# Kernel optimization log

Measured on AMD Instinct MI355X. Metric: run time of the kernel, lower is better.

Reference implementation:

```python
import jax, jax.numpy as jnp
import numpy as np

SHAPES = ((80, 80), (40, 40), (20, 20), (10, 10))  # (H, W) per level
N_HEADS = 8
N_POINTS = 4
D_MODEL = 512  # double_d_model = 2*256 (densefusion=True)
D_FFN = 1024
B = 2
L = len(SHAPES)
S = sum(h * w for h, w in SHAPES)  # 8500
EPS = 1e-5


def _layernorm(x, g, b):
    m = jnp.mean(x, axis=-1, keepdims=True)
    v = jnp.mean((x - m) ** 2, axis=-1, keepdims=True)
    return (x - m) * jax.lax.rsqrt(v + EPS) * g + b


def _reference_points(shapes):
    # encoder get_reference_points with valid_ratios == 1 -> [S, 2] (x, y) in (0,1)
    refs = []
    for (H, W) in shapes:
        ry = (jnp.arange(H, dtype=jnp.float32) + 0.5) / H
        rx = (jnp.arange(W, dtype=jnp.float32) + 0.5) / W
        gy, gx = jnp.meshgrid(ry, rx, indexing='ij')
        refs.append(jnp.stack([gx.reshape(-1), gy.reshape(-1)], axis=-1))
    return jnp.concatenate(refs, axis=0)


def _sample_level(val, loc, H, W):
    # val: [B, H*W, h, d]; loc: [B, S, h, P, 2] normalized in [0,1]
    b, _, h, d = val.shape
    s, p = loc.shape[1], loc.shape[3]
    x = loc[..., 0] * W - 0.5
    y = loc[..., 1] * H - 0.5
    x0 = jnp.floor(x)
    y0 = jnp.floor(y)
    wx = x - x0
    wy = y - y0
    x0i = x0.astype(jnp.int32)
    y0i = y0.astype(jnp.int32)

    def gather(xi, yi):
        valid = ((xi >= 0) & (xi < W) & (yi >= 0) & (yi < H)).astype(val.dtype)
        idx = jnp.clip(yi, 0, H - 1) * W + jnp.clip(xi, 0, W - 1)  # [B,S,h,P]
        idx2 = jnp.transpose(idx, (0, 1, 3, 2)).reshape(b, s * p, h)  # [B,S*P,h]
        g = jnp.take_along_axis(val, idx2[..., None], axis=1)  # [B,S*P,h,d]
        vmask = jnp.transpose(valid, (0, 1, 3, 2))[..., None]  # [B,S,P,h,1]
        return g.reshape(b, s, p, h, d) * vmask

    v00 = gather(x0i, y0i)
    v01 = gather(x0i + 1, y0i)
    v10 = gather(x0i, y0i + 1)
    v11 = gather(x0i + 1, y0i + 1)
    wxT = jnp.transpose(wx, (0, 1, 3, 2))[..., None]
    wyT = jnp.transpose(wy, (0, 1, 3, 2))[..., None]
    return (v00 * (1 - wxT) * (1 - wyT) + v01 * wxT * (1 - wyT)
            + v10 * (1 - wxT) * wyT + v11 * wxT * wyT)  # [B,S,P,h,d]


def _forward(src, pos, w_off, b_off, w_attn, b_attn, w_val, b_val, w_out, b_out,
             ln1_g, ln1_b, w1, b1, w2, b2, ln2_g, ln2_b, shapes):
    b, s, c = src.shape
    h, p, l = N_HEADS, N_POINTS, len(shapes)
    d = c // h
    q = src + pos
    value = (src @ w_val + b_val).reshape(b, s, h, d)
    offsets = (q @ w_off + b_off).reshape(b, s, h, l, p, 2)
    attn = jax.nn.softmax((q @ w_attn + b_attn).reshape(b, s, h, l * p), axis=-1)
    attn = attn.reshape(b, s, h, l, p)
    ref = _reference_points(shapes)  # [S,2]
    # offset normalizer = (W_l, H_l)
    norm = jnp.array([[W, H] for (H, W) in shapes], dtype=src.dtype)  # [L,2]
    loc = ref[None, :, None, None, None, :] + offsets / norm[None, None, None, :, None, :]
    # split value per level and sample
    starts = np.cumsum([0] + [H * W for (H, W) in shapes])[:-1]
    sampled = []
    for lvl, (H, W) in enumerate(shapes):
        val_l = jax.lax.dynamic_slice_in_dim(value, int(starts[lvl]), H * W, axis=1)
        sampled.append(_sample_level(val_l, loc[:, :, :, lvl], H, W))
    sampled = jnp.stack(sampled)  # [L,B,S,P,h,d]
    out = jnp.einsum('lbqphd,bqhlp->bqhd', sampled, attn).reshape(b, s, c)
    attn_out = out @ w_out + b_out
    x = _layernorm(src + attn_out, ln1_g, ln1_b)
    ffn = jax.nn.relu(x @ w1 + b1) @ w2 + b2
    return _layernorm(x + ffn, ln2_g, ln2_b)


def setup_inputs() -> dict:
    key = jax.random.key(0)
    ks = jax.random.split(key, 20)
    sc = 0.02
    C = D_MODEL
    hLP = N_HEADS * L * N_POINTS
    f32 = jnp.float32
    inp = {
        'src': jax.random.normal(ks[0], (B, S, C), f32),
        'pos': jax.random.normal(ks[1], (B, S, C), f32),
        'w_off': jax.random.normal(ks[2], (C, hLP * 2), f32) * sc,
        'b_off': jax.random.normal(ks[3], (hLP * 2,), f32) * sc,
        'w_attn': jax.random.normal(ks[4], (C, hLP), f32) * sc,
        'b_attn': jax.random.normal(ks[5], (hLP,), f32) * sc,
        'w_val': jax.random.normal(ks[6], (C, C), f32) * sc,
        'b_val': jnp.zeros((C,), f32),
        'w_out': jax.random.normal(ks[7], (C, C), f32) * sc,
        'b_out': jnp.zeros((C,), f32),
        'ln1_g': jnp.ones((C,), f32),
        'ln1_b': jnp.zeros((C,), f32),
        'w1': jax.random.normal(ks[8], (C, D_FFN), f32) * sc,
        'b1': jnp.zeros((D_FFN,), f32),
        'w2': jax.random.normal(ks[9], (D_FFN, C), f32) * sc,
        'b2': jnp.zeros((C,), f32),
        'ln2_g': jnp.ones((C,), f32),
        'ln2_b': jnp.zeros((C,), f32),
        'spatial_shapes': jnp.array(SHAPES, dtype=jnp.int32),
    }
    return inp


def reference(src, pos, w_off, b_off, w_attn, b_attn, w_val, b_val, w_out, b_out,
              ln1_g, ln1_b, w1, b1, w2, b2, ln2_g, ln2_b, spatial_shapes):
    shapes = tuple((int(a), int(b)) for a, b in np.asarray(spatial_shapes))
    return _forward(src, pos, w_off, b_off, w_attn, b_attn, w_val, b_val, w_out, b_out,
                    ln1_g, ln1_b, w1, b1, w2, b2, ln2_g, ln2_b, shapes)
```

## Files before the change

### kernel.cpp

```cpp
#include <hip/hip_runtime.h>


typedef __bf16 bf16_t;
typedef __bf16 bf16x8 __attribute__((ext_vector_type(8)));
typedef __bf16 bf16x4 __attribute__((ext_vector_type(4)));
typedef float  f32x4  __attribute__((ext_vector_type(4)));

#define M_ROWS 17000
#define S_LEN  8500

__device__ inline void store_c(float* p, float v)  { *p = v; }
__device__ inline void store_c(bf16_t* p, float v) { *p = (bf16_t)v; }

__device__ inline float4 load4f(const float* p)  { return *(const float4*)p; }
__device__ inline float4 load4f(const bf16_t* p) {
    bf16x4 v = *(const bf16x4*)p;
    return make_float4((float)v[0], (float)v[1], (float)v[2], (float)v[3]);
}

__global__ __launch_bounds__(256)
void transpose_kernel(const float* __restrict__ in, bf16_t* __restrict__ out,
                      int K, int N) {
    __shared__ float s[32][33];
    int tx = threadIdx.x & 31, ty = threadIdx.x >> 5;
    int k0 = blockIdx.x * 32, n0 = blockIdx.y * 32;
    #pragma unroll
    for (int i = 0; i < 4; i++)
        s[ty + 8 * i][tx] = in[(size_t)(k0 + ty + 8 * i) * N + n0 + tx];
    __syncthreads();
    #pragma unroll
    for (int i = 0; i < 4; i++)
        out[(size_t)(n0 + ty + 8 * i) * K + k0 + tx] = (bf16_t)s[tx][ty + 8 * i];
}

__global__ __launch_bounds__(384)
void prep_bias_kernel(const float* __restrict__ b_off, const float* __restrict__ b_attn,
                      float* __restrict__ bias_oa) {
    int i = threadIdx.x;
    bias_oa[i] = (i < 256) ? b_off[i] : b_attn[i - 256];
}

__global__ __launch_bounds__(256)
void add_q_kernel(const float* __restrict__ a, const float* __restrict__ b,
                  bf16_t* __restrict__ q, bf16_t* __restrict__ src_bf, int n4) {
    int i = blockIdx.x * 256 + threadIdx.x;
    if (i >= n4) return;
    float4 av = *(const float4*)(a + (size_t)i * 4);
    float4 bv = *(const float4*)(b + (size_t)i * 4);
    bf16x4 sv, ov;
    sv[0] = (bf16_t)av.x; sv[1] = (bf16_t)av.y; sv[2] = (bf16_t)av.z; sv[3] = (bf16_t)av.w;
    ov[0] = (bf16_t)(av.x + bv.x);
    ov[1] = (bf16_t)(av.y + bv.y);
    ov[2] = (bf16_t)(av.z + bv.z);
    ov[3] = (bf16_t)(av.w + bv.w);
    *(bf16x4*)(q      + (size_t)i * 4) = ov;
    *(bf16x4*)(src_bf + (size_t)i * 4) = sv;
}

template<typename OT, bool RELU>
__global__ __launch_bounds__(256)
void gemm128_kernel(const bf16_t* __restrict__ A, const bf16_t* __restrict__ Wt,
                    const float* __restrict__ bias, OT* __restrict__ Cout,
                    int M, int N, int K) {
    __shared__ bf16_t As[2][128][40];
    __shared__ bf16_t Bs[2][128][40];

    const int tid  = threadIdx.x;
    const int wave = tid >> 6;
    const int lane = tid & 63;
    const int quad = lane >> 4;
    const int lq   = lane & 15;
    const int wr   = (wave >> 1) * 64;
    const int wc   = (wave & 1) * 64;
    const int row0 = blockIdx.x * 128;
    const int col0 = blockIdx.y * 128;

    const int sr = tid >> 2;
    const int sc = (tid & 3) * 8;

    const bf16_t* gA0 = A  + (size_t)min(row0 + sr,      M - 1) * K + sc;
    const bf16_t* gA1 = A  + (size_t)min(row0 + sr + 64, M - 1) * K + sc;
    const bf16_t* gB0 = Wt + (size_t)(col0 + sr) * K + sc;
    const bf16_t* gB1 = Wt + (size_t)(col0 + sr + 64) * K + sc;

    f32x4 acc[4][4];
    #pragma unroll
    for (int i = 0; i < 4; i++)
        #pragma unroll
        for (int j = 0; j < 4; j++)
            #pragma unroll
            for (int r = 0; r < 4; r++) acc[i][j][r] = 0.f;

    bf16x8 pa0 = *(const bf16x8*)gA0;
    bf16x8 pa1 = *(const bf16x8*)gA1;
    bf16x8 pb0 = *(const bf16x8*)gB0;
    bf16x8 pb1 = *(const bf16x8*)gB1;

    const int nIter = K >> 5;
    for (int it = 0; it < nIter; it++) {
        const int cur = it & 1;
        *(bf16x8*)&As[cur][sr][sc]      = pa0;
        *(bf16x8*)&As[cur][sr + 64][sc] = pa1;
        *(bf16x8*)&Bs[cur][sr][sc]      = pb0;
        *(bf16x8*)&Bs[cur][sr + 64][sc] = pb1;
        __syncthreads();

        if (it + 1 < nIter) {
            int ko = (it + 1) << 5;
            pa0 = *(const bf16x8*)(gA0 + ko);
            pa1 = *(const bf16x8*)(gA1 + ko);
            pb0 = *(const bf16x8*)(gB0 + ko);
            pb1 = *(const bf16x8*)(gB1 + ko);
        }

        bf16x8 af[4], bfr[4];
        #pragma unroll
        for (int i = 0; i < 4; i++)
            af[i] = *(const bf16x8*)&As[cur][wr + i * 16 + lq][quad * 8];
        #pragma unroll
        for (int j = 0; j < 4; j++)
            bfr[j] = *(const bf16x8*)&Bs[cur][wc + j * 16 + lq][quad * 8];
        #pragma unroll
        for (int i = 0; i < 4; i++)
            #pragma unroll
            for (int j = 0; j < 4; j++)
                acc[i][j] = __builtin_amdgcn_mfma_f32_16x16x32_bf16(af[i], bfr[j], acc[i][j], 0, 0, 0);
    }

    #pragma unroll
    for (int j = 0; j < 4; j++) {
        int col = col0 + wc + j * 16 + lq;
        float bcol = bias[col];
        #pragma unroll
        for (int i = 0; i < 4; i++) {
            int rowb = row0 + wr + i * 16 + quad * 4;
            #pragma unroll
            for (int r = 0; r < 4; r++) {
                int row = rowb + r;
                if (row < M) {
                    float v = acc[i][j][r] + bcol;
                    if (RELU) v = fmaxf(v, 0.f);
                    store_c(Cout + (size_t)row * N + col, v);
                }
            }
        }
    }
}

__global__ __launch_bounds__(256)
void softmax16_kernel(float* __restrict__ oa, int ngroups) {
    int i = blockIdx.x * 256 + threadIdx.x;
    if (i >= ngroups) return;
    float* p = oa + (size_t)(i >> 3) * 384 + 256 + (i & 7) * 16;
    float v[16];
    float4* p4 = (float4*)p;
    #pragma unroll
    for (int j = 0; j < 4; j++) {
        float4 t = p4[j];
        v[4*j+0] = t.x; v[4*j+1] = t.y; v[4*j+2] = t.z; v[4*j+3] = t.w;
    }
    float mx = v[0];
    #pragma unroll
    for (int j = 1; j < 16; j++) mx = fmaxf(mx, v[j]);
    float sm = 0.f;
    #pragma unroll
    for (int j = 0; j < 16; j++) { v[j] = __expf(v[j] - mx); sm += v[j]; }
    float inv = 1.f / sm;
    #pragma unroll
    for (int j = 0; j < 4; j++)
        p4[j] = make_float4(v[4*j]*inv, v[4*j+1]*inv, v[4*j+2]*inv, v[4*j+3]*inv);
}

__global__ __launch_bounds__(256)
void sample_kernel(const bf16_t* __restrict__ value, const float* __restrict__ oa,
                   bf16_t* __restrict__ out) {
    int gw   = blockIdx.x * 4 + (threadIdx.x >> 6);
    int lane = threadIdx.x & 63;
    if (gw >= 2 * S_LEN * 8) return;
    int h  = gw & 7;
    int bs = gw >> 3;
    int b  = bs / S_LEN;
    int s  = bs - b * S_LEN;

    float rx, ry;
    if (s < 6400)      { int i = s;        float inv = 1.f/80.f; ry = ((i/80) + 0.5f)*inv; rx = ((i%80) + 0.5f)*inv; }
    else if (s < 8000) { int i = s - 6400; float inv = 1.f/40.f; ry = ((i/40) + 0.5f)*inv; rx = ((i%40) + 0.5f)*inv; }
    else if (s < 8400) { int i = s - 8000; float inv = 1.f/20.f; ry = ((i/20) + 0.5f)*inv; rx = ((i%20) + 0.5f)*inv; }
    else               { int i = s - 8400; float inv = 1.f/10.f; ry = ((i/10) + 0.5f)*inv; rx = ((i%10) + 0.5f)*inv; }

    const int WH[4]  = {80, 40, 20, 10};
    const int LST[4] = {0, 6400, 8000, 8400};

    int pt = lane >> 2;
    int cn = lane & 3;
    int ll = pt >> 2;
    int W  = WH[ll];
    const float* row = oa + (size_t)bs * 384;
    float2 o2 = *(const float2*)(row + h * 32 + pt * 2);
    float  aw = row[256 + h * 16 + pt];
    float x = fmaf(rx, (float)W, o2.x) - 0.5f;
    float y = fmaf(ry, (float)W, o2.y) - 0.5f;
    float fx = floorf(x), fy = floorf(y);
    float wx = x - fx,  wy = y - fy;
    int cx = (int)fx + (cn & 1);
    int cy = (int)fy + (cn >> 1);
    float wgt = aw * ((cn & 1) ? wx : 1.f - wx) * ((cn >> 1) ? wy : 1.f - wy);
    bool valid = (cx >= 0) && (cx < W) && (cy >= 0) && (cy < W);
    if (!valid) wgt = 0.f;
    int xc = min(max(cx, 0), W - 1);
    int yc = min(max(cy, 0), W - 1);
    int addr = LST[ll] + yc * W + xc;

    const bf16_t* vb = value + ((size_t)b * S_LEN) * 512 + h * 64 + (lane & 7) * 8;
    int sub = lane >> 3;
    float acc[8];
    #pragma unroll
    for (int j = 0; j < 8; j++) acc[j] = 0.f;
    #pragma unroll
    for (int it = 0; it < 8; it++) {
        int pair = it * 8 + sub;
        int   a = __shfl(addr, pair, 64);
        float w = __shfl(wgt,  pair, 64);
        bf16x8 v = *(const bf16x8*)(vb + (size_t)a * 512);
        #pragma unroll
        for (int j = 0; j < 8; j++) acc[j] += w * (float)v[j];
    }

    #pragma unroll
    for (int o = 8; o < 64; o <<= 1)
        #pragma unroll
        for (int j = 0; j < 8; j++) acc[j] += __shfl_xor(acc[j], o, 64);

    if (lane < 8) {
        bf16x8 ov;
        #pragma unroll
        for (int j = 0; j < 8; j++) ov[j] = (bf16_t)acc[j];
        *(bf16x8*)(out + (size_t)bs * 512 + h * 64 + lane * 8) = ov;
    }
}

template<typename INA, typename INB, typename OT>
__global__ __launch_bounds__(256)
void ln_kernel(const INA* __restrict__ Xa, const INB* __restrict__ Xb,
               const float* __restrict__ g, const float* __restrict__ be,
               OT* __restrict__ out, int M) {
    int wave = threadIdx.x >> 6;
    int lane = threadIdx.x & 63;
    int row = blockIdx.x * 4 + wave;
    if (row >= M) return;
    size_t base = (size_t)row * 512;
    float v[8];
    float s = 0.f, sq = 0.f;
    #pragma unroll
    for (int p = 0; p < 2; p++) {
        int idx = p * 256 + lane * 4;
        float4 a4 = load4f(Xa + base + idx);
        float4 b4 = load4f(Xb + base + idx);
        float t0 = a4.x + b4.x, t1 = a4.y + b4.y, t2 = a4.z + b4.z, t3 = a4.w + b4.w;
        v[p*4+0] = t0; v[p*4+1] = t1; v[p*4+2] = t2; v[p*4+3] = t3;
        s  += t0 + t1 + t2 + t3;
        sq += t0*t0 + t1*t1 + t2*t2 + t3*t3;
    }
    #pragma unroll
    for (int off = 32; off > 0; off >>= 1) {
        s  += __shfl_xor(s, off, 64);
        sq += __shfl_xor(sq, off, 64);
    }
    float mean = s * (1.f / 512.f);
    float var  = sq * (1.f / 512.f) - mean * mean;
    float rstd = rsqrtf(var + 1e-5f);
    #pragma unroll
    for (int p = 0; p < 2; p++) {
        int idx = p * 256 + lane * 4;
        #pragma unroll
        for (int j = 0; j < 4; j++) {
            int col = idx + j;
            float o = (v[p*4+j] - mean) * rstd * g[col] + be[col];
            store_c(out + base + col, o);
        }
    }
}

extern "C" void kernel_launch(void* const* d_in, const int* in_sizes, int n_in,
                              void* d_out, int out_size, void* d_ws, size_t ws_size,
                              hipStream_t stream) {
    const float* src    = (const float*)d_in[0];
    const float* pos    = (const float*)d_in[1];
    const float* w_off  = (const float*)d_in[2];
    const float* b_off  = (const float*)d_in[3];
    const float* w_attn = (const float*)d_in[4];
    const float* b_attn = (const float*)d_in[5];
    const float* w_val  = (const float*)d_in[6];
    const float* b_val  = (const float*)d_in[7];
    const float* w_out  = (const float*)d_in[8];
    const float* b_out  = (const float*)d_in[9];
    const float* ln1_g  = (const float*)d_in[10];
    const float* ln1_b  = (const float*)d_in[11];
    const float* w1     = (const float*)d_in[12];
    const float* b1     = (const float*)d_in[13];
    const float* w2     = (const float*)d_in[14];
    const float* b2     = (const float*)d_in[15];
    const float* ln2_g  = (const float*)d_in[16];
    const float* ln2_b  = (const float*)d_in[17];

    const int M = M_ROWS;
    char* ws = (char*)d_ws;
    size_t o = 0;
    auto alloc = [&](size_t bytes) { size_t r = o; o += (bytes + 255) & ~(size_t)255; return r; };

    size_t off_q       = alloc((size_t)M * 512 * 2);
    size_t off_srcbf   = alloc((size_t)M * 512 * 2);
    size_t off_value   = alloc((size_t)M * 512 * 2);
    size_t off_sampled = alloc((size_t)M * 512 * 2);
    size_t off_oa      = alloc((size_t)M * 384 * 4);
    size_t off_attnout = alloc((size_t)M * 512 * 2);
    size_t off_x       = alloc((size_t)M * 512 * 2);
    size_t off_wtval   = alloc((size_t)512 * 512 * 2);
    size_t off_wtoa    = alloc((size_t)384 * 512 * 2);
    size_t off_wtout   = alloc((size_t)512 * 512 * 2);
    size_t off_wtw1    = alloc((size_t)1024 * 512 * 2);
    size_t off_wtw2    = alloc((size_t)512 * 1024 * 2);
    size_t off_boa     = alloc((size_t)384 * 4);

    bf16_t* q        = (bf16_t*)(ws + off_q);
    bf16_t* src_bf   = (bf16_t*)(ws + off_srcbf);
    bf16_t* value    = (bf16_t*)(ws + off_value);
    bf16_t* sampled  = (bf16_t*)(ws + off_sampled);
    float*  oa       = (float*)(ws + off_oa);
    bf16_t* attn_out = (bf16_t*)(ws + off_attnout);
    bf16_t* x        = (bf16_t*)(ws + off_x);
    bf16_t* hidden   = (bf16_t*)(ws + off_sampled);
    bf16_t* ffn_out  = (bf16_t*)(ws + off_attnout);
    bf16_t* wt_val   = (bf16_t*)(ws + off_wtval);
    bf16_t* wt_oa    = (bf16_t*)(ws + off_wtoa);
    bf16_t* wt_out   = (bf16_t*)(ws + off_wtout);
    bf16_t* wt_w1    = (bf16_t*)(ws + off_wtw1);
    bf16_t* wt_w2    = (bf16_t*)(ws + off_wtw2);
    float*  bias_oa  = (float*)(ws + off_boa);
    float*  outp     = (float*)d_out;

    transpose_kernel<<<dim3(512/32,  512/32), 256, 0, stream>>>(w_val,  wt_val,  512,  512);
    transpose_kernel<<<dim3(512/32,  256/32), 256, 0, stream>>>(w_off,  wt_oa,   512,  256);
    transpose_kernel<<<dim3(512/32,  128/32), 256, 0, stream>>>(w_attn, wt_oa + (size_t)256*512, 512, 128);
    transpose_kernel<<<dim3(512/32,  512/32), 256, 0, stream>>>(w_out,  wt_out,  512,  512);
    transpose_kernel<<<dim3(512/32, 1024/32), 256, 0, stream>>>(w1,     wt_w1,   512, 1024);
    transpose_kernel<<<dim3(1024/32, 512/32), 256, 0, stream>>>(w2,     wt_w2,  1024,  512);
    prep_bias_kernel<<<1, 384, 0, stream>>>(b_off, b_attn, bias_oa);

    add_q_kernel<<<(M * 512 / 4 + 255) / 256, 256, 0, stream>>>(src, pos, q, src_bf, M * 512 / 4);

    const int MT = (M + 127) / 128;

    gemm128_kernel<bf16_t, false><<<dim3(MT, 4), 256, 0, stream>>>(src_bf, wt_val, b_val, value, M, 512, 512);
    gemm128_kernel<float,  false><<<dim3(MT, 3), 256, 0, stream>>>(q, wt_oa, bias_oa, oa, M, 384, 512);

    softmax16_kernel<<<(M * 8 + 255) / 256, 256, 0, stream>>>(oa, M * 8);

    sample_kernel<<<(M * 8) / 4, 256, 0, stream>>>(value, oa, sampled);

    gemm128_kernel<bf16_t, false><<<dim3(MT, 4), 256, 0, stream>>>(sampled, wt_out, b_out, attn_out, M, 512, 512);

    ln_kernel<float, bf16_t, bf16_t><<<(M + 3) / 4, 256, 0, stream>>>(src, attn_out, ln1_g, ln1_b, x, M);

    gemm128_kernel<bf16_t, true ><<<dim3(MT, 8), 256, 0, stream>>>(x, wt_w1, b1, hidden, M, 1024, 512);
    gemm128_kernel<bf16_t, false><<<dim3(MT, 4), 256, 0, stream>>>(hidden, wt_w2, b2, ffn_out, M, 512, 1024);

    ln_kernel<bf16_t, bf16_t, float><<<(M + 3) / 4, 256, 0, stream>>>(x, ffn_out, ln2_g, ln2_b, outp, M);
}
```

Baseline: 422.5 us.

## Use 32x32 MFMA tiles, merge value/offset GEMMs and fuse weight prep launches

Result: faster. 380.0 us (-10.0%).

```diff
diff --git a/kernel.cpp b/kernel.cpp
--- a/kernel.cpp
+++ b/kernel.cpp
@@ -5,6 +5,7 @@
 typedef __bf16 bf16x8 __attribute__((ext_vector_type(8)));
 typedef __bf16 bf16x4 __attribute__((ext_vector_type(4)));
 typedef float  f32x4  __attribute__((ext_vector_type(4)));
+typedef float  f32x16 __attribute__((ext_vector_type(16)));
 
 #define M_ROWS 17000
 #define S_LEN  8500
@@ -19,11 +20,34 @@
 }
 
 __global__ __launch_bounds__(256)
-void transpose_kernel(const float* __restrict__ in, bf16_t* __restrict__ out,
-                      int K, int N) {
+void prep_kernel(const float* __restrict__ w_val, const float* __restrict__ w_off,
+                 const float* __restrict__ w_attn, const float* __restrict__ w_out,
+                 const float* __restrict__ w1, const float* __restrict__ w2,
+                 const float* __restrict__ b_off, const float* __restrict__ b_attn,
+                 bf16_t* __restrict__ wt_val, bf16_t* __restrict__ wt_oa,
+                 bf16_t* __restrict__ wt_out, bf16_t* __restrict__ wt_w1,
+                 bf16_t* __restrict__ wt_w2, float* __restrict__ bias_oa) {
+    int z = blockIdx.z;
+    if (z == 6) {
+        if (blockIdx.x == 0 && blockIdx.y == 0) {
+            for (int i = threadIdx.x; i < 384; i += 256)
+                bias_oa[i] = (i < 256) ? b_off[i] : b_attn[i - 256];
+        }
+        return;
+    }
+    const float* in; bf16_t* out; int K, N;
+    switch (z) {
+        case 0: in = w_val;  out = wt_val;                     K = 512;  N = 512;  break;
+        case 1: in = w_off;  out = wt_oa;                      K = 512;  N = 256;  break;
+        case 2: in = w_attn; out = wt_oa + (size_t)256 * 512;  K = 512;  N = 128;  break;
+        case 3: in = w_out;  out = wt_out;                     K = 512;  N = 512;  break;
+        case 4: in = w1;     out = wt_w1;                      K = 512;  N = 1024; break;
+        default: in = w2;    out = wt_w2;                      K = 1024; N = 512;  break;
+    }
+    int k0 = blockIdx.x * 32, n0 = blockIdx.y * 32;
+    if (k0 >= K || n0 >= N) return;
     __shared__ float s[32][33];
     int tx = threadIdx.x & 31, ty = threadIdx.x >> 5;
-    int k0 = blockIdx.x * 32, n0 = blockIdx.y * 32;
     #pragma unroll
     for (int i = 0; i < 4; i++)
         s[ty + 8 * i][tx] = in[(size_t)(k0 + ty + 8 * i) * N + n0 + tx];
@@ -31,13 +55,6 @@
     #pragma unroll
     for (int i = 0; i < 4; i++)
         out[(size_t)(n0 + ty + 8 * i) * K + k0 + tx] = (bf16_t)s[tx][ty + 8 * i];
-}
-
-__global__ __launch_bounds__(384)
-void prep_bias_kernel(const float* __restrict__ b_off, const float* __restrict__ b_attn,
-                      float* __restrict__ bias_oa) {
-    int i = threadIdx.x;
-    bias_oa[i] = (i < 256) ? b_off[i] : b_attn[i - 256];
 }
 
 __global__ __launch_bounds__(256)
@@ -57,94 +74,125 @@
     *(bf16x4*)(src_bf + (size_t)i * 4) = sv;
 }
 
+#define GEMM_CORE(A_PTR, WT_PTR, K_DIM, EPILOGUE)                                  \
+    const int tid  = threadIdx.x;                                                  \
+    const int wave = tid >> 6;                                                     \
+    const int lane = tid & 63;                                                     \
+    const int l31  = lane & 31;                                                    \
+    const int lh8  = (lane >> 5) * 8;                                              \
+    const int wr   = (wave >> 1) * 64;                                             \
+    const int wc   = (wave & 1) * 64;                                              \
+    const int row0 = blockIdx.x * 128;                                             \
+    const int sr = tid >> 2;                                                       \
+    const int sc = (tid & 3) * 8;                                                  \
+    const bf16_t* gA0 = A_PTR  + (size_t)min(row0 + sr,      M_ROWS - 1) * K_DIM + sc; \
+    const bf16_t* gA1 = A_PTR  + (size_t)min(row0 + sr + 64, M_ROWS - 1) * K_DIM + sc; \
+    const bf16_t* gB0 = WT_PTR + (size_t)(col0 + sr) * K_DIM + sc;                 \
+    const bf16_t* gB1 = WT_PTR + (size_t)(col0 + sr + 64) * K_DIM + sc;            \
+    f32x16 acc[2][2];                                                              \
+    _Pragma("unroll")                                                              \
+    for (int i = 0; i < 2; i++)                                                    \
+        _Pragma("unroll")                                                          \
+        for (int j = 0; j < 2; j++)                                                \
+            _Pragma("unroll")                                                      \
+            for (int r = 0; r < 16; r++) acc[i][j][r] = 0.f;                       \
+    bf16x8 pa0 = *(const bf16x8*)gA0;                                              \
+    bf16x8 pa1 = *(const bf16x8*)gA1;                                              \
+    bf16x8 pb0 = *(const bf16x8*)gB0;                                              \
+    bf16x8 pb1 = *(const bf16x8*)gB1;                                              \
+    const int nIter = K_DIM >> 5;                                                  \
+    for (int it = 0; it < nIter; it++) {                                           \
+        const int cur = it & 1;                                                    \
+        *(bf16x8*)&As[cur][sr][sc]      = pa0;                                     \
+        *(bf16x8*)&As[cur][sr + 64][sc] = pa1;                                     \
+        *(bf16x8*)&Bs[cur][sr][sc]      = pb0;                                     \
+        *(bf16x8*)&Bs[cur][sr + 64][sc] = pb1;                                     \
+        __syncthreads();                                                           \
+        if (it + 1 < nIter) {                                                      \
+            int ko = (it + 1) << 5;                                                \
+            pa0 = *(const bf16x8*)(gA0 + ko);                                      \
+            pa1 = *(const bf16x8*)(gA1 + ko);                                      \
+            pb0 = *(const bf16x8*)(gB0 + ko);                                      \
+            pb1 = *(const bf16x8*)(gB1 + ko);                                      \
+        }                                                                          \
+        _Pragma("unroll")                                                          \
+        for (int kh = 0; kh < 2; kh++) {                                           \
+            bf16x8 a0 = *(const bf16x8*)&As[cur][wr + l31     ][kh * 16 + lh8];    \
+            bf16x8 a1 = *(const bf16x8*)&As[cur][wr + 32 + l31][kh * 16 + lh8];    \
+            bf16x8 b0 = *(const bf16x8*)&Bs[cur][wc + l31     ][kh * 16 + lh8];    \
+            bf16x8 b1 = *(const bf16x8*)&Bs[cur][wc + 32 + l31][kh * 16 + lh8];    \
+            acc[0][0] = __builtin_amdgcn_mfma_f32_32x32x16_bf16(a0, b0, acc[0][0], 0, 0, 0); \
+            acc[0][1] = __builtin_amdgcn_mfma_f32_32x32x16_bf16(a0, b1, acc[0][1], 0, 0, 0); \
+            acc[1][0] = __builtin_amdgcn_mfma_f32_32x32x16_bf16(a1, b0, acc[1][0], 0, 0, 0); \
+            acc[1][1] = __builtin_amdgcn_mfma_f32_32x32x16_bf16(a1, b1, acc[1][1], 0, 0, 0); \
+        }                                                                          \
+    }                                                                              \
+    EPILOGUE
+
 template<typename OT, bool RELU>
 __global__ __launch_bounds__(256)
 void gemm128_kernel(const bf16_t* __restrict__ A, const bf16_t* __restrict__ Wt,
                     const float* __restrict__ bias, OT* __restrict__ Cout,
-                    int M, int N, int K) {
+                    int N, int K) {
     __shared__ bf16_t As[2][128][40];
     __shared__ bf16_t Bs[2][128][40];
-
-    const int tid  = threadIdx.x;
-    const int wave = tid >> 6;
-    const int lane = tid & 63;
-    const int quad = lane >> 4;
-    const int lq   = lane & 15;
-    const int wr   = (wave >> 1) * 64;
-    const int wc   = (wave & 1) * 64;
-    const int row0 = blockIdx.x * 128;
     const int col0 = blockIdx.y * 128;
-
-    const int sr = tid >> 2;
-    const int sc = (tid & 3) * 8;
-
-    const bf16_t* gA0 = A  + (size_t)min(row0 + sr,      M - 1) * K + sc;
-    const bf16_t* gA1 = A  + (size_t)min(row0 + sr + 64, M - 1) * K + sc;
-    const bf16_t* gB0 = Wt + (size_t)(col0 + sr) * K + sc;
-    const bf16_t* gB1 = Wt + (size_t)(col0 + sr + 64) * K + sc;
-
-    f32x4 acc[4][4];
-    #pragma unroll
-    for (int i = 0; i < 4; i++)
-        #pragma unroll
-        for (int j = 0; j < 4; j++)
-            #pragma unroll
-            for (int r = 0; r < 4; r++) acc[i][j][r] = 0.f;
-
-    bf16x8 pa0 = *(const bf16x8*)gA0;
-    bf16x8 pa1 = *(const bf16x8*)gA1;
-    bf16x8 pb0 = *(const bf16x8*)gB0;
-    bf16x8 pb1 = *(const bf16x8*)gB1;
-
-    const int nIter = K >> 5;
-    for (int it = 0; it < nIter; it++) {
-        const int cur = it & 1;
-        *(bf16x8*)&As[cur][sr][sc]      = pa0;
-        *(bf16x8*)&As[cur][sr + 64][sc] = pa1;
-        *(bf16x8*)&Bs[cur][sr][sc]      = pb0;
-        *(bf16x8*)&Bs[cur][sr + 64][sc] = pb1;
-        __syncthreads();
-
-        if (it + 1 < nIter) {
-            int ko = (it + 1) << 5;
-            pa0 = *(const bf16x8*)(gA0 + ko);
-            pa1 = *(const bf16x8*)(gA1 + ko);
-            pb0 = *(const bf16x8*)(gB0 + ko);
-            pb1 = *(const bf16x8*)(gB1 + ko);
+    GEMM_CORE(A, Wt, K,
+        {
+            _Pragma("unroll")
+            for (int i = 0; i < 2; i++)
+                _Pragma("unroll")
+                for (int j = 0; j < 2; j++) {
+                    int col = col0 + wc + j * 32 + l31;
+                    float bcol = bias[col];
+                    _Pragma("unroll")
+                    for (int reg = 0; reg < 16; reg++) {
+                        int row = row0 + wr + i * 32 + (reg & 3) + 8 * (reg >> 2) + 4 * (lane >> 5);
+                        if (row < M_ROWS) {
+                            float v = acc[i][j][reg] + bcol;
+                            if (RELU) v = fmaxf(v, 0.f);
+                            store_c(Cout + (size_t)row * N + col, v);
+                        }
+                    }
+                }
         }
-
-        bf16x8 af[4], bfr[4];
-        #pragma unroll
-        for (int i = 0; i < 4; i++)
-            af[i] = *(const bf16x8*)&As[cur][wr + i * 16 + lq][quad * 8];
-        #pragma unroll
-        for (int j = 0; j < 4; j++)
-            bfr[j] = *(const bf16x8*)&Bs[cur][wc + j * 16 + lq][quad * 8];
-        #pragma unroll
-        for (int i = 0; i < 4; i++)
-            #pragma unroll
-            for (int j = 0; j < 4; j++)
-                acc[i][j] = __builtin_amdgcn_mfma_f32_16x16x32_bf16(af[i], bfr[j], acc[i][j], 0, 0, 0);
-    }
-
-    #pragma unroll
-    for (int j = 0; j < 4; j++) {
-        int col = col0 + wc + j * 16 + lq;
-        float bcol = bias[col];
-        #pragma unroll
-        for (int i = 0; i < 4; i++) {
-            int rowb = row0 + wr + i * 16 + quad * 4;
-            #pragma unroll
-            for (int r = 0; r < 4; r++) {
-                int row = rowb + r;
-                if (row < M) {
-                    float v = acc[i][j][r] + bcol;
-                    if (RELU) v = fmaxf(v, 0.f);
-                    store_c(Cout + (size_t)row * N + col, v);
+    )
+}
+
+__global__ __launch_bounds__(256)
+void gemm_voa_kernel(const bf16_t* __restrict__ src_bf, const bf16_t* __restrict__ q,
+                     const bf16_t* __restrict__ wt_val, const bf16_t* __restrict__ wt_oa,
+                     const float* __restrict__ b_val, const float* __restrict__ bias_oa,
+                     bf16_t* __restrict__ value, float* __restrict__ oa) {
+    __shared__ bf16_t As[2][128][40];
+    __shared__ bf16_t Bs[2][128][40];
+    const int by    = blockIdx.y;
+    const bool isV  = by < 4;
+    const int col0  = (isV ? by : by - 4) * 128;
+    const bf16_t* Ap  = isV ? src_bf : q;
+    const bf16_t* Wp  = isV ? wt_val : wt_oa;
+    const float* bp   = isV ? b_val : bias_oa;
+    const int Nout    = isV ? 512 : 384;
+    GEMM_CORE(Ap, Wp, 512,
+        {
+            _Pragma("unroll")
+            for (int i = 0; i < 2; i++)
+                _Pragma("unroll")
+                for (int j = 0; j < 2; j++) {
+                    int col = col0 + wc + j * 32 + l31;
+                    float bcol = bp[col];
+                    _Pragma("unroll")
+                    for (int reg = 0; reg < 16; reg++) {
+                        int row = row0 + wr + i * 32 + (reg & 3) + 8 * (reg >> 2) + 4 * (lane >> 5);
+                        if (row < M_ROWS) {
+                            float v = acc[i][j][reg] + bcol;
+                            if (isV) value[(size_t)row * 512 + col] = (bf16_t)v;
+                            else     oa[(size_t)row * 384 + col] = v;
+                        }
+                    }
                 }
-            }
         }
-    }
+    )
 }
 
 __global__ __launch_bounds__(256)
@@ -225,7 +273,6 @@
         #pragma unroll
         for (int j = 0; j < 8; j++) acc[j] += w * (float)v[j];
     }
-
     #pragma unroll
     for (int o = 8; o < 64; o <<= 1)
         #pragma unroll
@@ -339,31 +386,26 @@
     float*  bias_oa  = (float*)(ws + off_boa);
     float*  outp     = (float*)d_out;
 
-    transpose_kernel<<<dim3(512/32,  512/32), 256, 0, stream>>>(w_val,  wt_val,  512,  512);
-    transpose_kernel<<<dim3(512/32,  256/32), 256, 0, stream>>>(w_off,  wt_oa,   512,  256);
-    transpose_kernel<<<dim3(512/32,  128/32), 256, 0, stream>>>(w_attn, wt_oa + (size_t)256*512, 512, 128);
-    transpose_kernel<<<dim3(512/32,  512/32), 256, 0, stream>>>(w_out,  wt_out,  512,  512);
-    transpose_kernel<<<dim3(512/32, 1024/32), 256, 0, stream>>>(w1,     wt_w1,   512, 1024);
-    transpose_kernel<<<dim3(1024/32, 512/32), 256, 0, stream>>>(w2,     wt_w2,  1024,  512);
-    prep_bias_kernel<<<1, 384, 0, stream>>>(b_off, b_attn, bias_oa);
+    prep_kernel<<<dim3(32, 32, 7), 256, 0, stream>>>(
+        w_val, w_off, w_attn, w_out, w1, w2, b_off, b_attn,
+        wt_val, wt_oa, wt_out, wt_w1, wt_w2, bias_oa);
 
     add_q_kernel<<<(M * 512 / 4 + 255) / 256, 256, 0, stream>>>(src, pos, q, src_bf, M * 512 / 4);
 
     const int MT = (M + 127) / 128;
 
-    gemm128_kernel<bf16_t, false><<<dim3(MT, 4), 256, 0, stream>>>(src_bf, wt_val, b_val, value, M, 512, 512);
-    gemm128_kernel<float,  false><<<dim3(MT, 3), 256, 0, stream>>>(q, wt_oa, bias_oa, oa, M, 384, 512);
+    gemm_voa_kernel<<<dim3(MT, 7), 256, 0, stream>>>(src_bf, q, wt_val, wt_oa, b_val, bias_oa, value, oa);
 
     softmax16_kernel<<<(M * 8 + 255) / 256, 256, 0, stream>>>(oa, M * 8);
 
     sample_kernel<<<(M * 8) / 4, 256, 0, stream>>>(value, oa, sampled);
 
-    gemm128_kernel<bf16_t, false><<<dim3(MT, 4), 256, 0, stream>>>(sampled, wt_out, b_out, attn_out, M, 512, 512);
+    gemm128_kernel<bf16_t, false><<<dim3(MT, 4), 256, 0, stream>>>(sampled, wt_out, b_out, attn_out, 512, 512);
 
     ln_kernel<float, bf16_t, bf16_t><<<(M + 3) / 4, 256, 0, stream>>>(src, attn_out, ln1_g, ln1_b, x, M);
 
-    gemm128_kernel<bf16_t, true ><<<dim3(MT, 8), 256, 0, stream>>>(x, wt_w1, b1, hidden, M, 1024, 512);
-    gemm128_kernel<bf16_t, false><<<dim3(MT, 4), 256, 0, stream>>>(hidden, wt_w2, b2, ffn_out, M, 512, 1024);
+    gemm128_kernel<bf16_t, true ><<<dim3(MT, 8), 256, 0, stream>>>(x, wt_w1, b1, hidden, 1024, 512);
+    gemm128_kernel<bf16_t, false><<<dim3(MT, 4), 256, 0, stream>>>(hidden, wt_w2, b2, ffn_out, 512, 1024);
 
     ln_kernel<bf16_t, bf16_t, float><<<(M + 3) / 4, 256, 0, stream>>>(x, ffn_out, ln2_g, ln2_b, outp, M);
 }
```
